# Kernel tuning notes

Hardware: AMD Instinct MI355X
Metric: run time of the kernel (lower is better)

## Reference

```python
import jax, jax.numpy as jnp
from jax import lax
import numpy as np

B, N, C, P = 8, 512, 256, 7
CQ = C // 4
NMS_THRESH = 0.5
BBOX_XFORM_CLIP = 4.135166556742356  # log(1000/16)


def setup_inputs():
    key = jax.random.key(0)
    ks = jax.random.split(key, 24)
    rn = lambda k, s, sc=0.02: jax.random.normal(k, s, jnp.float32) * sc
    box_feats_q = jax.random.normal(ks[0], (B, N, C, P, P), jnp.float32)
    box_feats_s = jax.random.normal(ks[1], (B, 1, C, P, P), jnp.float32)
    xy = jax.random.uniform(ks[2], (B, N, 2), jnp.float32, 0.0, 700.0)
    wh = jax.random.uniform(ks[3], (B, N, 2), jnp.float32, 8.0, 96.0)
    proposals = jnp.concatenate([xy, xy + wh], axis=-1)  # [B,N,4] valid x1y1x2y2
    image_size = jnp.array([800, 800], jnp.int32)  # (H, W)
    return {
        'box_feats_q': box_feats_q, 'box_feats_s': box_feats_s,
        'proposals': proposals, 'image_size': image_size,
        'W1': rn(ks[4], (CQ, 2 * C)),          # conv1 1x1: 2C -> C/4
        'W2': rn(ks[5], (CQ, CQ, 3, 3)),       # conv2 3x3 valid
        'W3': rn(ks[6], (C, CQ)),              # conv3 1x1: C/4 -> C
        'Wcor': rn(ks[7], (C, C)),             # conv_cor 1x1
        'fc1_w': rn(ks[8], (C, 2 * C)), 'fc1_b': jnp.zeros((C,), jnp.float32),
        'fc2_w': rn(ks[9], (C, C)), 'fc2_b': jnp.zeros((C,), jnp.float32),
        'sfc_w': rn(ks[10], (1, C)), 'sfc_b': jnp.zeros((1,), jnp.float32),
        'scor_w': rn(ks[11], (1, C)), 'scor_b': jnp.zeros((1,), jnp.float32),
        'spr_w': rn(ks[12], (1, C)), 'spr_b': jnp.zeros((1,), jnp.float32),
        'dpr_w': rn(ks[13], (4, C)), 'dpr_b': jnp.zeros((4,), jnp.float32),
    }


def avgpool3(x):  # AvgPool2d(3, stride=1), NCHW
    s = lax.reduce_window(x, 0.0, lax.add, (1, 1, 3, 3), (1, 1, 1, 1), 'VALID')
    return s / 9.0


def head_forward(box_feats_q, box_feats_s, W1, W2, W3, Wcor, fc1_w, fc1_b, fc2_w,
                 fc2_b, sfc_w, sfc_b, scor_w, scor_b, spr_w, spr_b, dpr_w, dpr_b):
    M = B * N
    x_q = box_feats_q.reshape(M, C, P, P)
    x_s = jnp.broadcast_to(box_feats_s, (B, N, C, P, P)).reshape(M, C, P, P)
    # FC branch (avgpool_fc == global mean over 7x7)
    x_fc = jnp.concatenate([x_q.mean((2, 3)), x_s.mean((2, 3))], axis=1)  # [M,2C]
    h = jax.nn.relu(x_fc @ fc1_w.T + fc1_b)
    h = jax.nn.relu(h @ fc2_w.T + fc2_b)
    score_fc = h @ sfc_w.T + sfc_b  # [M,1]
    # Correlation branch: grouped 7x7 conv == per-channel spatial dot product
    x_cor_q = jnp.einsum('oc,mchw->mohw', Wcor, x_q)
    x_cor_s = jnp.einsum('oc,mchw->mohw', Wcor, x_s)
    x_relu = jax.nn.relu((x_cor_q * x_cor_s).sum((2, 3)))  # [M,C]
    score_cor = x_relu @ scor_w.T + scor_b  # [M,1]
    # Conv branch
    x = jnp.concatenate([x_q, x_s], axis=1)                    # [M,2C,7,7]
    x = jax.nn.relu(jnp.einsum('oc,mchw->mohw', W1, x))        # [M,CQ,7,7]
    x = avgpool3(x)                                            # [M,CQ,5,5]
    x = jax.nn.relu(lax.conv_general_dilated(x, W2, (1, 1), 'VALID',
        dimension_numbers=('NCHW', 'OIHW', 'NCHW')))           # [M,CQ,3,3]
    x = jax.nn.relu(jnp.einsum('oc,mchw->mohw', W3, x))        # [M,C,3,3]
    x = avgpool3(x).squeeze(3).squeeze(2)                      # [M,C]
    score_pr = x @ spr_w.T + spr_b
    pred_scores = score_pr + score_cor + score_fc              # [M,1]
    pred_deltas = x @ dpr_w.T + dpr_b                          # [M,4]
    return pred_scores, pred_deltas


def decode_boxes(deltas, boxes):
    w = boxes[:, 2] - boxes[:, 0]
    h = boxes[:, 3] - boxes[:, 1]
    cx = boxes[:, 0] + 0.5 * w
    cy = boxes[:, 1] + 0.5 * h
    dx, dy = deltas[:, 0], deltas[:, 1]
    dw = jnp.minimum(deltas[:, 2], BBOX_XFORM_CLIP)
    dh = jnp.minimum(deltas[:, 3], BBOX_XFORM_CLIP)
    pcx, pcy = dx * w + cx, dy * h + cy
    pw, ph = jnp.exp(dw) * w, jnp.exp(dh) * h
    return jnp.stack([pcx - 0.5 * pw, pcy - 0.5 * ph,
                      pcx + 0.5 * pw, pcy + 0.5 * ph], axis=1)


def nms_mask(boxes, scores, thresh):  # fixed-shape NMS -> keep mask [n]
    n = boxes.shape[0]
    order = jnp.argsort(-scores)
    b = boxes[order]
    area = jnp.maximum(b[:, 2] - b[:, 0], 0) * jnp.maximum(b[:, 3] - b[:, 1], 0)
    idx = jnp.arange(n)

    def body(i, keep):
        x1 = jnp.maximum(b[i, 0], b[:, 0]); y1 = jnp.maximum(b[i, 1], b[:, 1])
        x2 = jnp.minimum(b[i, 2], b[:, 2]); y2 = jnp.minimum(b[i, 3], b[:, 3])
        inter = jnp.maximum(x2 - x1, 0) * jnp.maximum(y2 - y1, 0)
        iou = inter / jnp.maximum(area[i] + area - inter, 1e-9)
        suppress = (iou > thresh) & (idx > i) & keep[i]
        return keep & ~suppress

    keep_sorted = lax.fori_loop(0, n, body, jnp.ones((n,), bool))
    return jnp.zeros((n,), bool).at[order].set(keep_sorted)


def reference(box_feats_q, box_feats_s, proposals, image_size, W1, W2, W3, Wcor,
              fc1_w, fc1_b, fc2_w, fc2_b, sfc_w, sfc_b, scor_w, scor_b,
              spr_w, spr_b, dpr_w, dpr_b):
    pred_scores, pred_deltas = head_forward(
        box_feats_q, box_feats_s, W1, W2, W3, Wcor, fc1_w, fc1_b, fc2_w, fc2_b,
        sfc_w, sfc_b, scor_w, scor_b, spr_w, spr_b, dpr_w, dpr_b)
    M = B * N
    # decode on detached deltas
    pred_boxes = decode_boxes(lax.stop_gradient(pred_deltas), proposals.reshape(M, 4))
    H = image_size[0].astype(jnp.float32)
    W_ = image_size[1].astype(jnp.float32)
    pred_boxes = jnp.stack([
        jnp.clip(pred_boxes[:, 0], 0.0, W_), jnp.clip(pred_boxes[:, 1], 0.0, H),
        jnp.clip(pred_boxes[:, 2], 0.0, W_), jnp.clip(pred_boxes[:, 3], 0.0, H)],
        axis=1).reshape(B, N, 4)
    scores = jax.nn.sigmoid(lax.stop_gradient(pred_scores)).reshape(B, N)
    keep = jax.vmap(lambda bx, sc: nms_mask(bx, sc, NMS_THRESH))(pred_boxes, scores)
    # boxes/scores padded to fixed [B,N,...]; keep mask marks NMS survivors
    return pred_boxes, scores, keep
```

## Files before the change

kernel.cpp:

```cpp
#include <hip/hip_runtime.h>
#include <math.h>

typedef float f4 __attribute__((ext_vector_type(4)));
typedef f4 f4u __attribute__((aligned(4)));
typedef float f32x4 __attribute__((ext_vector_type(4)));
typedef short short8 __attribute__((ext_vector_type(8)));

constexpr int NB  = 8;
constexpr int NN  = 512;
constexpr int NC  = 256;
constexpr int NHW = 49;
constexpr int NM  = NB * NN;
constexpr int XS  = 260;

constexpr size_t WS_SMEAN = 0;
constexpr size_t WS_YST   = 2048;
constexpr size_t WS_UST   = 102400;
constexpr size_t WS_WFH   = 127488;
constexpr size_t WS_WFL   = 168448;
constexpr size_t WS_SP    = 209408;
constexpr size_t WS_QMEAN = 213504;
constexpr size_t WS_SBOX  = WS_QMEAN;
constexpr size_t WS_SAREA = WS_SBOX + 16384;
constexpr size_t WS_SIDX  = WS_SAREA + 4096;
constexpr size_t WS_MASK  = WS_SIDX + 4096;

constexpr size_t OUT_SCORES = (size_t)NM * 4;
constexpr size_t OUT_KEEP   = OUT_SCORES + NM;

__device__ __forceinline__ float block_reduce_sum(float v, float* red) {
    int t = threadIdx.x;
#pragma unroll
    for (int off = 32; off > 0; off >>= 1) v += __shfl_down(v, off, 64);
    __syncthreads();
    if ((t & 63) == 0) red[t >> 6] = v;
    __syncthreads();
    return red[0] + red[1] + red[2] + red[3];
}

__device__ __forceinline__ unsigned short bf16_rne(float f) {
    unsigned u = __float_as_uint(f);
    return (unsigned short)((u + 0x7FFFu + ((u >> 16) & 1u)) >> 16);
}
__device__ __forceinline__ float bf16_to_f(unsigned short h) {
    return __uint_as_float(((unsigned)h) << 16);
}

__device__ __forceinline__ void stage_xT(const float* __restrict__ g, float* sx, int t) {
#pragma unroll
    for (int rep = 0; rep < 13; ++rep) {
        int id = rep * 256 + t;
        if (id < 3136) {
            int c4 = id / 49;
            int hw = id - c4 * 49;
            f4 v;
            v[0] = g[(c4 * 4 + 0) * 49 + hw];
            v[1] = g[(c4 * 4 + 1) * 49 + hw];
            v[2] = g[(c4 * 4 + 2) * 49 + hw];
            v[3] = g[(c4 * 4 + 3) * 49 + hw];
            *(f4*)&sx[hw * XS + c4 * 4] = v;
        }
    }
}

__global__ __launch_bounds__(256, 2) void k_prep(
    const float* __restrict__ bfs, const float* __restrict__ Wcor,
    const float* __restrict__ W1, float* __restrict__ ws)
{
    int t = threadIdx.x, blk = blockIdx.x;

    if (blk >= 64) {
        int ob = (blk - 64) * 4 + (t >> 6);
        int l = t & 63;
        int mt = ob >> 3, ks = ob & 7;
        int row = mt * 16 + (l & 15);
        int k0 = ks * 32 + (l >> 4) * 8;
        const float* src = (row < 256) ? (Wcor + (size_t)row * 256 + k0)
                                       : (W1 + (size_t)(row - 256) * 512 + k0);
        short hv[8], lv[8];
#pragma unroll
        for (int j = 0; j < 8; ++j) {
            float v = src[j];
            unsigned short hh = bf16_rne(v);
            unsigned short hl = bf16_rne(v - bf16_to_f(hh));
            hv[j] = (short)hh; lv[j] = (short)hl;
        }
        short* dh = (short*)(ws + WS_WFH) + ((size_t)ob * 64 + l) * 8;
        short* dl = (short*)(ws + WS_WFL) + ((size_t)ob * 64 + l) * 8;
#pragma unroll
        for (int j = 0; j < 8; ++j) { dh[j] = hv[j]; dl[j] = lv[j]; }
        return;
    }

    __shared__ __align__(16) float smem[49 * XS + 16];
    float* sx = smem;
    int b = blk >> 3;
    int og8 = blk & 7;

    stage_xT(bfs + (size_t)b * 12544, sx, t);
    __syncthreads();

    if (og8 == 0) {
        float s = 0.f;
        for (int hw = 0; hw < 49; ++hw) s += sx[hw * XS + t];
        ws[WS_SMEAN + (size_t)b * 256 + t] = s * (1.f / 49.f);
    }

    int og2 = t >> 3, hwg = t & 7;
    int hwb = (hwg == 7) ? 0 : hwg * 7;
    int oA = og8 * 32 + og2;
    bool do_u = (og8 < 2);
    int o2 = og8 * 32 + og2;

    float acc0[7] = {0,0,0,0,0,0,0};
    float a1a[7]  = {0,0,0,0,0,0,0};
    const float* xrow = sx + hwb * XS;
    const float* w0r = Wcor + (size_t)oA * 256;
    const float* war = W1 + (size_t)o2 * 512 + 256;

#pragma unroll 1
    for (int c4 = 0; c4 < 64; ++c4) {
        f4 xv[7];
#pragma unroll
        for (int i = 0; i < 7; ++i) xv[i] = *(const f4*)&xrow[i * XS + c4 * 4];
        f4 w0 = *(const f4*)&w0r[c4 * 4];
        f4 wa = *(const f4*)&war[c4 * 4];
#pragma unroll
        for (int j = 0; j < 4; ++j) {
#pragma unroll
            for (int i = 0; i < 7; ++i) {
                float x = xv[i][j];
                acc0[i] = fmaf(w0[j], x, acc0[i]);
                a1a[i]  = fmaf(wa[j], x, a1a[i]);
            }
        }
    }

    if (hwg < 7) {
#pragma unroll
        for (int i = 0; i < 7; ++i) {
            int hw = hwb + i;
            ws[WS_YST + ((size_t)b * 256 + oA) * 49 + hw] = acc0[i];
            if (do_u)
                ws[WS_UST + ((size_t)b * 64 + o2) * 49 + hw] = a1a[i];
        }
    }
}

__global__ __launch_bounds__(256, 3) void k_heavy(
    const float* __restrict__ bfq,
    const float* __restrict__ W2, const float* __restrict__ W3,
    const float* __restrict__ scor_w, const float* __restrict__ scor_b,
    const float* __restrict__ spr_w, const float* __restrict__ spr_b,
    const float* __restrict__ dpr_w, const float* __restrict__ dpr_b,
    const float* __restrict__ proposals, const int* __restrict__ image_size,
    float* __restrict__ ws, float* __restrict__ out)
{
    __shared__ __align__(16) short xh[49 * 256];
    __shared__ __align__(16) short xl[49 * 256];
    __shared__ float red[20];

    int t = threadIdx.x, m = blockIdx.x, b = m >> 9;
    const float* xg = bfq + (size_t)m * 12544 + (size_t)t * 49;

    {
        float qs = 0.f;
#pragma unroll
        for (int r = 0; r < 12; ++r) {
            f4u v = *(const f4u*)&xg[r * 4];
#pragma unroll
            for (int j = 0; j < 4; ++j) {
                int hw = r * 4 + j;
                float x = v[j];
                qs += x;
                unsigned short hh = bf16_rne(x);
                int idx = (hw * 256 + t) ^ ((hw & 7) << 3);
                xh[idx] = (short)hh;
                xl[idx] = (short)bf16_rne(x - bf16_to_f(hh));
            }
        }
        float x48 = xg[48];
        qs += x48;
        unsigned short hh48 = bf16_rne(x48);
        xh[48 * 256 + t] = (short)hh48;
        xl[48 * 256 + t] = (short)bf16_rne(x48 - bf16_to_f(hh48));
        ws[WS_QMEAN + (size_t)m * 256 + t] = qs * (1.f / 49.f);
    }
    __syncthreads();

    int w = t >> 6, l = t & 63, cl = l & 15, g = l >> 4;

    f32x4 acc[5][4];
#pragma unroll
    for (int i = 0; i < 5; ++i)
#pragma unroll
        for (int nt = 0; nt < 4; ++nt) acc[i][nt] = (f32x4)0.f;

    const short* wfH = (const short*)(ws + WS_WFH);
    const short* wfL = (const short*)(ws + WS_WFL);

    int bcol[4];
#pragma unroll
    for (int nt = 0; nt < 4; ++nt) {
        int col = nt * 16 + cl;
        if (col >= 49) col = 0;
        bcol[nt] = col;
    }

#pragma unroll 1
    for (int ks = 0; ks < 8; ++ks) {
        short8 bh[4], bl[4];
#pragma unroll
        for (int nt = 0; nt < 4; ++nt) {
            int col = bcol[nt];
            int idx = (col * 256 + ks * 32 + g * 8) ^ ((col & 7) << 3);
            bh[nt] = *(const short8*)&xh[idx];
            bl[nt] = *(const short8*)&xl[idx];
        }
#pragma unroll
        for (int i = 0; i < 5; ++i) {
            int mt = w + 4 * i;
            size_t off = ((size_t)(mt * 8 + ks) * 64 + l) * 8;
            short8 ah = *(const short8*)&wfH[off];
            short8 al = *(const short8*)&wfL[off];
            acc[i][0] = __builtin_amdgcn_mfma_f32_16x16x32_bf16(ah, bh[0], acc[i][0], 0, 0, 0);
            acc[i][1] = __builtin_amdgcn_mfma_f32_16x16x32_bf16(ah, bh[1], acc[i][1], 0, 0, 0);
            acc[i][2] = __builtin_amdgcn_mfma_f32_16x16x32_bf16(ah, bh[2], acc[i][2], 0, 0, 0);
            acc[i][3] = __builtin_amdgcn_mfma_f32_16x16x32_bf16(ah, bh[3], acc[i][3], 0, 0, 0);
            acc[i][0] = __builtin_amdgcn_mfma_f32_16x16x32_bf16(ah, bl[0], acc[i][0], 0, 0, 0);
            acc[i][1] = __builtin_amdgcn_mfma_f32_16x16x32_bf16(ah, bl[1], acc[i][1], 0, 0, 0);
            acc[i][2] = __builtin_amdgcn_mfma_f32_16x16x32_bf16(ah, bl[2], acc[i][2], 0, 0, 0);
            acc[i][3] = __builtin_amdgcn_mfma_f32_16x16x32_bf16(ah, bl[3], acc[i][3], 0, 0, 0);
            acc[i][0] = __builtin_amdgcn_mfma_f32_16x16x32_bf16(al, bh[0], acc[i][0], 0, 0, 0);
            acc[i][1] = __builtin_amdgcn_mfma_f32_16x16x32_bf16(al, bh[1], acc[i][1], 0, 0, 0);
            acc[i][2] = __builtin_amdgcn_mfma_f32_16x16x32_bf16(al, bh[2], acc[i][2], 0, 0, 0);
            acc[i][3] = __builtin_amdgcn_mfma_f32_16x16x32_bf16(al, bh[3], acc[i][3], 0, 0, 0);
        }
    }

    float csum = 0.f;
    {
        const float* yb = ws + WS_YST + (size_t)b * 256 * 49;
#pragma unroll
        for (int i = 0; i < 4; ++i) {
            int row0 = (w + 4 * i) * 16 + g * 4;
#pragma unroll
            for (int q = 0; q < 4; ++q) {
                int row = row0 + q;
                float p = 0.f;
#pragma unroll
                for (int nt = 0; nt < 4; ++nt) {
                    int col = nt * 16 + cl;
                    if (col < 49) p += acc[i][nt][q] * yb[(size_t)row * 49 + col];
                }
                p += __shfl_xor(p, 1, 64);
                p += __shfl_xor(p, 2, 64);
                p += __shfl_xor(p, 4, 64);
                p += __shfl_xor(p, 8, 64);
                if (cl == 0) csum += fmaxf(p, 0.f) * scor_w[row];
            }
        }
    }
    __syncthreads();

    float* s1    = (float*)xh;
    float* sp1   = s1 + 64 * 52;
    float* cpart = (float*)xl;
    float* sc2T  = cpart + 2816;
    {
        const float* ub = ws + WS_UST + (size_t)b * 64 * 49;
        int ch0 = w * 16 + g * 4;
#pragma unroll
        for (int q = 0; q < 4; ++q) {
            int ch = ch0 + q;
#pragma unroll
            for (int nt = 0; nt < 4; ++nt) {
                int col = nt * 16 + cl;
                if (col < 49)
                    s1[ch * 52 + col] = fmaxf(acc[4][nt][q] + ub[(size_t)ch * 49 + col], 0.f);
            }
        }
    }
    __syncthreads();

    for (int i = t; i < 64 * 25; i += 256) {
        int ch = i / 25, pos = i - ch * 25;
        int py = pos / 5, px = pos - py * 5;
        const float* base = s1 + ch * 52 + py * 7 + px;
        float s = base[0] + base[1] + base[2]
                + base[7] + base[8] + base[9]
                + base[14] + base[15] + base[16];
        sp1[ch * 28 + pos] = s * (1.f / 9.f);
    }
    __syncthreads();

    {
        int oc = t & 63, icq = t >> 6;
        float a9[9] = {0,0,0,0,0,0,0,0,0};
        const float* wb2 = W2 + (size_t)oc * 576 + icq * 16 * 9;
#pragma unroll 1
        for (int ic16 = 0; ic16 < 16; ++ic16) {
            int ic = icq * 16 + ic16;
            const f4* ar = (const f4*)(sp1 + ic * 28);
            float av[28];
            *(f4*)&av[0]  = ar[0];
            *(f4*)&av[4]  = ar[1];
            *(f4*)&av[8]  = ar[2];
            *(f4*)&av[12] = ar[3];
            *(f4*)&av[16] = ar[4];
            *(f4*)&av[20] = ar[5];
            *(f4*)&av[24] = ar[6];
            const float* wi = wb2 + ic16 * 9;
            f4u w0 = *(const f4u*)wi;
            f4u w1 = *(const f4u*)(wi + 4);
            float wv[9] = { w0[0], w0[1], w0[2], w0[3], w1[0], w1[1], w1[2], w1[3], wi[8] };
#pragma unroll
            for (int py = 0; py < 3; ++py)
#pragma unroll
                for (int px = 0; px < 3; ++px) {
                    int p9 = py * 3 + px;
#pragma unroll
                    for (int ky = 0; ky < 3; ++ky)
#pragma unroll
                        for (int kx = 0; kx < 3; ++kx)
                            a9[p9] = fmaf(wv[ky * 3 + kx],
                                          av[(py + ky) * 5 + (px + kx)], a9[p9]);
                }
        }
#pragma unroll
        for (int p = 0; p < 9; ++p)
            cpart[((size_t)icq * 64 + oc) * 11 + p] = a9[p];
    }
    __syncthreads();

    for (int i = t; i < 576; i += 256) {
        int pos = i >> 6, occ = i & 63;
        float s = cpart[((size_t)0 * 64 + occ) * 11 + pos]
                + cpart[((size_t)1 * 64 + occ) * 11 + pos]
                + cpart[((size_t)2 * 64 + occ) * 11 + pos]
                + cpart[((size_t)3 * 64 + occ) * 11 + pos];
        sc2T[pos * 64 + occ] = fmaxf(s, 0.f);
    }
    __syncthreads();

    float xfin;
    {
        float xw[9] = {0,0,0,0,0,0,0,0,0};
        const f4* wr = (const f4*)(W3 + (size_t)t * 64);
#pragma unroll 1
        for (int gg = 0; gg < 16; ++gg) {
            f4 wv4 = wr[gg];
#pragma unroll
            for (int p = 0; p < 9; ++p) {
                f4 c = *(const f4*)(sc2T + p * 64 + gg * 4);
                xw[p] = fmaf(wv4[0], c[0], xw[p]);
                xw[p] = fmaf(wv4[1], c[1], xw[p]);
                xw[p] = fmaf(wv4[2], c[2], xw[p]);
                xw[p] = fmaf(wv4[3], c[3], xw[p]);
            }
        }
        float s = 0.f;
#pragma unroll
        for (int p = 0; p < 9; ++p) s += fmaxf(xw[p], 0.f);
        xfin = s * (1.f / 9.f);
    }

    float v0 = xfin * spr_w[t] + csum;
    float v1 = xfin * dpr_w[0 * 256 + t];
    float v2 = xfin * dpr_w[1 * 256 + t];
    float v3 = xfin * dpr_w[2 * 256 + t];
    float v4 = xfin * dpr_w[3 * 256 + t];
#pragma unroll
    for (int off = 32; off > 0; off >>= 1) {
        v0 += __shfl_xor(v0, off, 64);
        v1 += __shfl_xor(v1, off, 64);
        v2 += __shfl_xor(v2, off, 64);
        v3 += __shfl_xor(v3, off, 64);
        v4 += __shfl_xor(v4, off, 64);
    }
    if (l == 0) {
        red[w * 5 + 0] = v0; red[w * 5 + 1] = v1; red[w * 5 + 2] = v2;
        red[w * 5 + 3] = v3; red[w * 5 + 4] = v4;
    }
    __syncthreads();

    if (t == 0) {
        float r_s  = red[0] + red[5] + red[10] + red[15];
        float r_d0 = red[1] + red[6] + red[11] + red[16];
        float r_d1 = red[2] + red[7] + red[12] + red[17];
        float r_d2 = red[3] + red[8] + red[13] + red[18];
        float r_d3 = red[4] + red[9] + red[14] + red[19];

        ws[WS_SP + m] = r_s + spr_b[0] + scor_b[0];

        float d0 = r_d0 + dpr_b[0];
        float d1 = r_d1 + dpr_b[1];
        float d2 = fminf(r_d2 + dpr_b[2], 4.135166556742356f);
        float d3 = fminf(r_d3 + dpr_b[3], 4.135166556742356f);

        const float* pr = proposals + (size_t)m * 4;
        float x1p = pr[0], y1p = pr[1], x2p = pr[2], y2p = pr[3];
        float wd = x2p - x1p, hd = y2p - y1p;
        float cx = x1p + 0.5f * wd, cy = y1p + 0.5f * hd;
        float pcx = d0 * wd + cx, pcy = d1 * hd + cy;
        float pw = expf(d2) * wd, ph = expf(d3) * hd;
        float Wf = (float)image_size[1];
        float Hf = (float)image_size[0];
        out[(size_t)m * 4 + 0] = fminf(fmaxf(pcx - 0.5f * pw, 0.f), Wf);
        out[(size_t)m * 4 + 1] = fminf(fmaxf(pcy - 0.5f * ph, 0.f), Hf);
        out[(size_t)m * 4 + 2] = fminf(fmaxf(pcx + 0.5f * pw, 0.f), Wf);
        out[(size_t)m * 4 + 3] = fminf(fmaxf(pcy + 0.5f * ph, 0.f), Hf);
    }
}

__global__ __launch_bounds__(256) void k_fc(
    const float* __restrict__ fc1_w, const float* __restrict__ fc1_b,
    const float* __restrict__ fc2_w, const float* __restrict__ fc2_b,
    const float* __restrict__ sfc_w, const float* __restrict__ sfc_b,
    float* __restrict__ ws, float* __restrict__ out)
{
    __shared__ __align__(16) float sxfc[8][512];
    __shared__ __align__(16) float sh1[8][256];
    __shared__ float s_red[8];
    int t = threadIdx.x;
    int m0 = blockIdx.x * 8;

#pragma unroll
    for (int mi = 0; mi < 8; ++mi) {
        int mg = m0 + mi;
        int b = mg >> 9;
        sxfc[mi][t]       = ws[WS_QMEAN + (size_t)mg * 256 + t];
        sxfc[mi][256 + t] = ws[WS_SMEAN + (size_t)b * 256 + t];
    }
    __syncthreads();

    {
        const f4* wr = (const f4*)(fc1_w + t * 512);
        float acc[8] = {0,0,0,0,0,0,0,0};
        for (int k4 = 0; k4 < 128; ++k4) {
            f4 w = wr[k4];
#pragma unroll
            for (int mi = 0; mi < 8; ++mi) {
                f4 x = ((const f4*)sxfc[mi])[k4];
                acc[mi] = fmaf(w[0], x[0], acc[mi]);
                acc[mi] = fmaf(w[1], x[1], acc[mi]);
                acc[mi] = fmaf(w[2], x[2], acc[mi]);
                acc[mi] = fmaf(w[3], x[3], acc[mi]);
            }
        }
        float bb = fc1_b[t];
#pragma unroll
        for (int mi = 0; mi < 8; ++mi) sh1[mi][t] = fmaxf(acc[mi] + bb, 0.f);
    }
    __syncthreads();

    float val[8];
    {
        const f4* wr = (const f4*)(fc2_w + t * 256);
        float acc[8] = {0,0,0,0,0,0,0,0};
        for (int k4 = 0; k4 < 64; ++k4) {
            f4 w = wr[k4];
#pragma unroll
            for (int mi = 0; mi < 8; ++mi) {
                f4 x = ((const f4*)sh1[mi])[k4];
                acc[mi] = fmaf(w[0], x[0], acc[mi]);
                acc[mi] = fmaf(w[1], x[1], acc[mi]);
                acc[mi] = fmaf(w[2], x[2], acc[mi]);
                acc[mi] = fmaf(w[3], x[3], acc[mi]);
            }
        }
        float bb = fc2_b[t];
        float sw = sfc_w[t];
#pragma unroll
        for (int mi = 0; mi < 8; ++mi) val[mi] = sw * fmaxf(acc[mi] + bb, 0.f);
    }

#pragma unroll
    for (int mi = 0; mi < 8; ++mi) {
        float r = block_reduce_sum(val[mi], s_red);
        if (t == 0) {
            float tot = ws[WS_SP + m0 + mi] + (r + sfc_b[0]);
            out[OUT_SCORES + m0 + mi] = 1.0f / (1.0f + expf(-tot));
        }
    }
}

__global__ __launch_bounds__(256) void k_sort(
    const float* __restrict__ out, float* __restrict__ ws)
{
    __shared__ float ssc[512];
    int t = threadIdx.x, b = blockIdx.x;
    const float* sc_g = out + OUT_SCORES + (size_t)b * 512;
    ssc[t] = sc_g[t];
    ssc[t + 256] = sc_g[t + 256];
    __syncthreads();

#pragma unroll
    for (int ii = 0; ii < 2; ++ii) {
        int i = t + ii * 256;
        float si = ssc[i];
        int r = 0;
        for (int j = 0; j < 512; ++j) {
            float sj = ssc[j];
            r += (int)((sj > si) || (sj == si && j < i));
        }
        f4 v = *(const f4*)(out + ((size_t)b * 512 + i) * 4);
        *(f4*)&ws[WS_SBOX + ((size_t)b * 512 + r) * 4] = v;
        ws[WS_SAREA + (size_t)b * 512 + r] =
            fmaxf(v[2] - v[0], 0.f) * fmaxf(v[3] - v[1], 0.f);
        ((int*)ws)[WS_SIDX + (size_t)b * 512 + r] = i;
    }
}

__global__ __launch_bounds__(256) void k_mask(float* __restrict__ ws)
{
    int t = threadIdx.x;
    int wv = t >> 6, lane = t & 63;
    int gi = blockIdx.x * 4 + wv;
    int b = gi >> 9, i = gi & 511;

    f4 bi = *(const f4*)&ws[WS_SBOX + ((size_t)b * 512 + i) * 4];
    float ai = ws[WS_SAREA + (size_t)b * 512 + i];
    unsigned long long* mask = (unsigned long long*)(ws + WS_MASK);

#pragma unroll
    for (int w = 0; w < 8; ++w) {
        int j = w * 64 + lane;
        f4 bj = *(const f4*)&ws[WS_SBOX + ((size_t)b * 512 + j) * 4];
        float aj = ws[WS_SAREA + (size_t)b * 512 + j];
        float xx1 = fmaxf(bi[0], bj[0]), yy1 = fmaxf(bi[1], bj[1]);
        float xx2 = fminf(bi[2], bj[2]), yy2 = fminf(bi[3], bj[3]);
        float inter = fmaxf(xx2 - xx1, 0.f) * fmaxf(yy2 - yy1, 0.f);
        float iou = inter / fmaxf(ai + aj - inter, 1e-9f);
        bool sup = (iou > 0.5f) && (j > i);
        unsigned long long bal = __ballot(sup);
        if (lane == 0) mask[((size_t)b * 512 + i) * 8 + w] = bal;
    }
}

__global__ __launch_bounds__(64) void k_final(
    float* __restrict__ out, const float* __restrict__ wsf)
{
    int lane = threadIdx.x, b = blockIdx.x;
    const unsigned long long* mask =
        (const unsigned long long*)(wsf + WS_MASK) + (size_t)b * 512 * 8;

    unsigned long long kw = ~0ull;
    unsigned long long nxt = (lane < 8) ? mask[lane] : 0ull;

    for (int i = 0; i < 512; ++i) {
        unsigned long long cur = nxt;
        if (i < 511 && lane < 8) nxt = mask[(size_t)(i + 1) * 8 + lane];
        unsigned long long wi = __shfl(kw, i >> 6, 64);
        if ((wi >> (i & 63)) & 1ull) {
            if (lane < 8) kw &= ~cur;
        }
    }

    const int* sidx = ((const int*)wsf) + WS_SIDX + (size_t)b * 512;
#pragma unroll
    for (int w = 0; w < 8; ++w) {
        unsigned long long word = __shfl(kw, w, 64);
        int r = w * 64 + lane;
        out[OUT_KEEP + (size_t)b * 512 + sidx[r]] =
            ((word >> lane) & 1ull) ? 1.0f : 0.0f;
    }
}

extern "C" void kernel_launch(void* const* d_in, const int* in_sizes, int n_in,
                              void* d_out, int out_size, void* d_ws, size_t ws_size,
                              hipStream_t stream) {
    const float* bfq       = (const float*)d_in[0];
    const float* bfs       = (const float*)d_in[1];
    const float* proposals = (const float*)d_in[2];
    const int*   image_sz  = (const int*)d_in[3];
    const float* W1        = (const float*)d_in[4];
    const float* W2        = (const float*)d_in[5];
    const float* W3        = (const float*)d_in[6];
    const float* Wcor      = (const float*)d_in[7];
    const float* fc1_w     = (const float*)d_in[8];
    const float* fc1_b     = (const float*)d_in[9];
    const float* fc2_w     = (const float*)d_in[10];
    const float* fc2_b     = (const float*)d_in[11];
    const float* sfc_w     = (const float*)d_in[12];
    const float* sfc_b     = (const float*)d_in[13];
    const float* scor_w    = (const float*)d_in[14];
    const float* scor_b    = (const float*)d_in[15];
    const float* spr_w     = (const float*)d_in[16];
    const float* spr_b     = (const float*)d_in[17];
    const float* dpr_w     = (const float*)d_in[18];
    const float* dpr_b     = (const float*)d_in[19];
    float* out = (float*)d_out;
    float* ws  = (float*)d_ws;

    k_prep<<<104, 256, 0, stream>>>(bfs, Wcor, W1, ws);
    k_heavy<<<NM, 256, 0, stream>>>(bfq, W2, W3,
                                    scor_w, scor_b, spr_w, spr_b,
                                    dpr_w, dpr_b, proposals, image_sz, ws, out);
    k_fc<<<NM / 8, 256, 0, stream>>>(fc1_w, fc1_b, fc2_w, fc2_b,
                                     sfc_w, sfc_b, ws, out);
    k_sort<<<NB, 256, 0, stream>>>(out, ws);
    k_mask<<<1024, 256, 0, stream>>>(ws);
    k_final<<<NB, 64, 0, stream>>>(out, ws);
}
```

Before: 494.6 us.

## Fuse FC branch into heavy per-proposal kernel and drop k_fc launch

Computes the fc1/fc2/score FC branch inside k_heavy, one proposal per block, using the in-register query mean and the shared-memory buffer s1, then folds the FC score into the existing block reduction and writes the sigmoid score directly. This removes the k_fc launch and the workspace round trip for query means and partial scores. In exchange, each block streams the full fc1/fc2 weights (about 768 KB) once per proposal instead of once per 8 proposals, so weight traffic goes up about 8x (mostly L2 hits), and the heavy kernel gets longer and may use more registers.

```diff
diff --git a/kernel.cpp b/kernel.cpp
--- a/kernel.cpp
+++ b/kernel.cpp
@@ -18,25 +18,14 @@
 constexpr size_t WS_UST   = 102400;
 constexpr size_t WS_WFH   = 127488;
 constexpr size_t WS_WFL   = 168448;
-constexpr size_t WS_SP    = 209408;
-constexpr size_t WS_QMEAN = 213504;
-constexpr size_t WS_SBOX  = WS_QMEAN;
+constexpr size_t WS_NMS   = 209408;
+constexpr size_t WS_SBOX  = WS_NMS;
 constexpr size_t WS_SAREA = WS_SBOX + 16384;
 constexpr size_t WS_SIDX  = WS_SAREA + 4096;
 constexpr size_t WS_MASK  = WS_SIDX + 4096;
 
 constexpr size_t OUT_SCORES = (size_t)NM * 4;
 constexpr size_t OUT_KEEP   = OUT_SCORES + NM;
-
-__device__ __forceinline__ float block_reduce_sum(float v, float* red) {
-    int t = threadIdx.x;
-#pragma unroll
-    for (int off = 32; off > 0; off >>= 1) v += __shfl_down(v, off, 64);
-    __syncthreads();
-    if ((t & 63) == 0) red[t >> 6] = v;
-    __syncthreads();
-    return red[0] + red[1] + red[2] + red[3];
-}
 
 __device__ __forceinline__ unsigned short bf16_rne(float f) {
     unsigned u = __float_as_uint(f);
@@ -153,6 +142,9 @@
     const float* __restrict__ scor_w, const float* __restrict__ scor_b,
     const float* __restrict__ spr_w, const float* __restrict__ spr_b,
     const float* __restrict__ dpr_w, const float* __restrict__ dpr_b,
+    const float* __restrict__ fc1_w, const float* __restrict__ fc1_b,
+    const float* __restrict__ fc2_w, const float* __restrict__ fc2_b,
+    const float* __restrict__ sfc_w, const float* __restrict__ sfc_b,
     const float* __restrict__ proposals, const int* __restrict__ image_size,
     float* __restrict__ ws, float* __restrict__ out)
 {
@@ -163,8 +155,8 @@
     int t = threadIdx.x, m = blockIdx.x, b = m >> 9;
     const float* xg = bfq + (size_t)m * 12544 + (size_t)t * 49;
 
-    {
-        float qs = 0.f;
+    float q_sum = 0.f;
+    {
 #pragma unroll
         for (int r = 0; r < 12; ++r) {
             f4u v = *(const f4u*)&xg[r * 4];
@@ -172,7 +164,7 @@
             for (int j = 0; j < 4; ++j) {
                 int hw = r * 4 + j;
                 float x = v[j];
-                qs += x;
+                q_sum += x;
                 unsigned short hh = bf16_rne(x);
                 int idx = (hw * 256 + t) ^ ((hw & 7) << 3);
                 xh[idx] = (short)hh;
@@ -180,11 +172,10 @@
             }
         }
         float x48 = xg[48];
-        qs += x48;
+        q_sum += x48;
         unsigned short hh48 = bf16_rne(x48);
         xh[48 * 256 + t] = (short)hh48;
         xl[48 * 256 + t] = (short)bf16_rne(x48 - bf16_to_f(hh48));
-        ws[WS_QMEAN + (size_t)m * 256 + t] = qs * (1.f / 49.f);
     }
     __syncthreads();
 
@@ -365,7 +356,44 @@
         xfin = s * (1.f / 9.f);
     }
 
-    float v0 = xfin * spr_w[t] + csum;
+    float* xfc  = s1;
+    float* hbuf = s1 + 512;
+    xfc[t]       = q_sum * (1.f / 49.f);
+    xfc[256 + t] = ws[WS_SMEAN + (size_t)b * 256 + t];
+    __syncthreads();
+
+    float fcval;
+    {
+        const f4* wr = (const f4*)(fc1_w + (size_t)t * 512);
+        float a = 0.f;
+#pragma unroll 1
+        for (int k4 = 0; k4 < 128; ++k4) {
+            f4 wv = wr[k4];
+            f4 xv = *(const f4*)&xfc[k4 * 4];
+            a = fmaf(wv[0], xv[0], a);
+            a = fmaf(wv[1], xv[1], a);
+            a = fmaf(wv[2], xv[2], a);
+            a = fmaf(wv[3], xv[3], a);
+        }
+        hbuf[t] = fmaxf(a + fc1_b[t], 0.f);
+    }
+    __syncthreads();
+    {
+        const f4* wr = (const f4*)(fc2_w + (size_t)t * 256);
+        float a = 0.f;
+#pragma unroll 1
+        for (int k4 = 0; k4 < 64; ++k4) {
+            f4 wv = wr[k4];
+            f4 xv = *(const f4*)&hbuf[k4 * 4];
+            a = fmaf(wv[0], xv[0], a);
+            a = fmaf(wv[1], xv[1], a);
+            a = fmaf(wv[2], xv[2], a);
+            a = fmaf(wv[3], xv[3], a);
+        }
+        fcval = sfc_w[t] * fmaxf(a + fc2_b[t], 0.f);
+    }
+
+    float v0 = xfin * spr_w[t] + csum + fcval;
     float v1 = xfin * dpr_w[0 * 256 + t];
     float v2 = xfin * dpr_w[1 * 256 + t];
     float v3 = xfin * dpr_w[2 * 256 + t];
@@ -391,7 +419,8 @@
         float r_d2 = red[3] + red[8] + red[13] + red[18];
         float r_d3 = red[4] + red[9] + red[14] + red[19];
 
-        ws[WS_SP + m] = r_s + spr_b[0] + scor_b[0];
+        float tot = r_s + spr_b[0] + scor_b[0] + sfc_b[0];
+        out[OUT_SCORES + m] = 1.0f / (1.0f + expf(-tot));
 
         float d0 = r_d0 + dpr_b[0];
         float d1 = r_d1 + dpr_b[1];
@@ -410,78 +439,6 @@
         out[(size_t)m * 4 + 1] = fminf(fmaxf(pcy - 0.5f * ph, 0.f), Hf);
         out[(size_t)m * 4 + 2] = fminf(fmaxf(pcx + 0.5f * pw, 0.f), Wf);
         out[(size_t)m * 4 + 3] = fminf(fmaxf(pcy + 0.5f * ph, 0.f), Hf);
-    }
-}
-
-__global__ __launch_bounds__(256) void k_fc(
-    const float* __restrict__ fc1_w, const float* __restrict__ fc1_b,
-    const float* __restrict__ fc2_w, const float* __restrict__ fc2_b,
-    const float* __restrict__ sfc_w, const float* __restrict__ sfc_b,
-    float* __restrict__ ws, float* __restrict__ out)
-{
-    __shared__ __align__(16) float sxfc[8][512];
-    __shared__ __align__(16) float sh1[8][256];
-    __shared__ float s_red[8];
-    int t = threadIdx.x;
-    int m0 = blockIdx.x * 8;
-
-#pragma unroll
-    for (int mi = 0; mi < 8; ++mi) {
-        int mg = m0 + mi;
-        int b = mg >> 9;
-        sxfc[mi][t]       = ws[WS_QMEAN + (size_t)mg * 256 + t];
-        sxfc[mi][256 + t] = ws[WS_SMEAN + (size_t)b * 256 + t];
-    }
-    __syncthreads();
-
-    {
-        const f4* wr = (const f4*)(fc1_w + t * 512);
-        float acc[8] = {0,0,0,0,0,0,0,0};
-        for (int k4 = 0; k4 < 128; ++k4) {
-            f4 w = wr[k4];
-#pragma unroll
-            for (int mi = 0; mi < 8; ++mi) {
-                f4 x = ((const f4*)sxfc[mi])[k4];
-                acc[mi] = fmaf(w[0], x[0], acc[mi]);
-                acc[mi] = fmaf(w[1], x[1], acc[mi]);
-                acc[mi] = fmaf(w[2], x[2], acc[mi]);
-                acc[mi] = fmaf(w[3], x[3], acc[mi]);
-            }
-        }
-        float bb = fc1_b[t];
-#pragma unroll
-        for (int mi = 0; mi < 8; ++mi) sh1[mi][t] = fmaxf(acc[mi] + bb, 0.f);
-    }
-    __syncthreads();
-
-    float val[8];
-    {
-        const f4* wr = (const f4*)(fc2_w + t * 256);
-        float acc[8] = {0,0,0,0,0,0,0,0};
-        for (int k4 = 0; k4 < 64; ++k4) {
-            f4 w = wr[k4];
-#pragma unroll
-            for (int mi = 0; mi < 8; ++mi) {
-                f4 x = ((const f4*)sh1[mi])[k4];
-                acc[mi] = fmaf(w[0], x[0], acc[mi]);
-                acc[mi] = fmaf(w[1], x[1], acc[mi]);
-                acc[mi] = fmaf(w[2], x[2], acc[mi]);
-                acc[mi] = fmaf(w[3], x[3], acc[mi]);
-            }
-        }
-        float bb = fc2_b[t];
-        float sw = sfc_w[t];
-#pragma unroll
-        for (int mi = 0; mi < 8; ++mi) val[mi] = sw * fmaxf(acc[mi] + bb, 0.f);
-    }
-
-#pragma unroll
-    for (int mi = 0; mi < 8; ++mi) {
-        float r = block_reduce_sum(val[mi], s_red);
-        if (t == 0) {
-            float tot = ws[WS_SP + m0 + mi] + (r + sfc_b[0]);
-            out[OUT_SCORES + m0 + mi] = 1.0f / (1.0f + expf(-tot));
-        }
     }
 }
 
@@ -596,9 +553,9 @@
     k_prep<<<104, 256, 0, stream>>>(bfs, Wcor, W1, ws);
     k_heavy<<<NM, 256, 0, stream>>>(bfq, W2, W3,
                                     scor_w, scor_b, spr_w, spr_b,
-                                    dpr_w, dpr_b, proposals, image_sz, ws, out);
-    k_fc<<<NM / 8, 256, 0, stream>>>(fc1_w, fc1_b, fc2_w, fc2_b,
-                                     sfc_w, sfc_b, ws, out);
+                                    dpr_w, dpr_b,
+                                    fc1_w, fc1_b, fc2_w, fc2_b, sfc_w, sfc_b,
+                                    proposals, image_sz, ws, out);
     k_sort<<<NB, 256, 0, stream>>>(out, ws);
     k_mask<<<1024, 256, 0, stream>>>(ws);
     k_final<<<NB, 64, 0, stream>>>(out, ws);
```

Measured after the change: 1.151 ms. 133% more time.
